# Performance work log

Hardware: AMD Instinct MI355X
Metric: run time of the kernel (lower is better)

## Reference

```python
import jax, jax.numpy as jnp
import numpy as np

B, A, E = 16384, 8, 512


def setup_inputs() -> dict:
    key = jax.random.key(0)
    ks = jax.random.split(key, 6)
    return {
        "image_features": jax.random.normal(ks[0], (B, E), dtype=jnp.float32),
        "edge_attributes": jax.random.normal(ks[1], (B, A, E), dtype=jnp.float32),
        "linear_w": jax.random.normal(ks[2], (E, 2 * E), dtype=jnp.float32) * (1.0 / np.sqrt(2 * E)),
        "linear_b": jax.random.normal(ks[3], (E,), dtype=jnp.float32) * 0.01,
        "fwd_proj": jax.random.normal(ks[4], (A, E, E), dtype=jnp.float32) * (1.0 / np.sqrt(E)),
        "bwd_proj": jax.random.normal(ks[5], (A, E, E), dtype=jnp.float32) * (1.0 / np.sqrt(E)),
        "self_weighted": jnp.ones((1, A, 1), dtype=jnp.float32),
    }


def reference(image_features, edge_attributes, linear_w, linear_b, fwd_proj, bwd_proj, self_weighted):
    # Forward attribute GNN: broadcast src over attribute axis, concat, linear(2E->E)
    src = jnp.broadcast_to(image_features[:, None, :], edge_attributes.shape)  # [B,A,E]
    x = jnp.concatenate([src, edge_attributes], axis=-1)                       # [B,A,2E]
    agg = jnp.einsum('bak,ek->bae', x, linear_w) + linear_b                    # [B,A,E]
    attr_rep = jnp.einsum('bai,aij->baj', agg, fwd_proj)                       # [B,A,E]

    # Backward attribute GNN: per-type projection, ReLU, learned weighted sum over A
    proj = jnp.einsum('bai,aij->baj', attr_rep, bwd_proj)                      # [B,A,E]
    individuals = jnp.sum(jax.nn.relu(proj) * self_weighted, axis=1)           # [B,E]
    return attr_rep, individuals
```

## Files before the change

### kernel.cpp

```cpp
#include <hip/hip_runtime.h>
#include <cstdint>
#include <cstddef>

#define NB 16384
#define NA 8
#define NE 512
#define NK 1024
#define NN 4096

typedef __bf16 bf16x8 __attribute__((ext_vector_type(8)));
typedef float  f32x4  __attribute__((ext_vector_type(4)));
typedef uint16_t u16x8 __attribute__((ext_vector_type(8)));

__device__ __forceinline__ uint16_t cvt_bf16(float f) {
    uint32_t u = __builtin_bit_cast(uint32_t, f);
    u += 0x7fffu + ((u >> 16) & 1u);
    return (uint16_t)(u >> 16);
}

__device__ __forceinline__ int swz(int row) { return (row ^ (row >> 2)) & 3; }

__device__ __forceinline__ void gl_lds16(const void* g, void* l) {
    __builtin_amdgcn_global_load_lds(
        (__attribute__((address_space(1))) void*)(void*)g,
        (__attribute__((address_space(3))) void*)l, 16, 0, 0);
}

__global__ __launch_bounds__(256) void k_tcvt(const float* __restrict__ in,
                                              uint16_t* __restrict__ out,
                                              int R, int C) {
    __shared__ float tile[32][33];
    int mat = blockIdx.z;
    int c0 = blockIdx.x * 32, r0 = blockIdx.y * 32;
    int tx = threadIdx.x & 31, ty = threadIdx.x >> 5;
    const float* src = in + (size_t)mat * R * C;
    uint16_t* dst = out + (size_t)mat * R * C;
#pragma unroll
    for (int yy = 0; yy < 4; ++yy) {
        int r = ty + yy * 8;
        tile[r][tx] = src[(size_t)(r0 + r) * C + c0 + tx];
    }
    __syncthreads();
#pragma unroll
    for (int yy = 0; yy < 4; ++yy) {
        int c = ty + yy * 8;
        dst[(size_t)(c0 + c) * R + r0 + tx] = cvt_bf16(tile[tx][c]);
    }
}

__global__ __launch_bounds__(256) void k_cvt4(const float* __restrict__ in,
                                              uint16_t* __restrict__ out, int n4) {
    int i = blockIdx.x * 256 + threadIdx.x;
    if (i >= n4) return;
    float4 v = ((const float4*)in)[i];
    ushort4 o;
    o.x = cvt_bf16(v.x); o.y = cvt_bf16(v.y); o.z = cvt_bf16(v.z); o.w = cvt_bf16(v.w);
    ((ushort4*)out)[i] = o;
}

__global__ __launch_bounds__(256) void k_bvec(const float* __restrict__ lb,
                                              const float* __restrict__ fwd,
                                              float* __restrict__ bvec) {
    int a = blockIdx.x >> 4, i0 = (blockIdx.x & 15) * 32;
    int t = threadIdx.x;
    float s0 = 0.f, s1 = 0.f;
#pragma unroll 4
    for (int i = 0; i < 32; ++i) {
        float w = lb[i0 + i];
        const float* f = fwd + ((size_t)a * NE + i0 + i) * NE;
        s0 = fmaf(w, f[t], s0);
        s1 = fmaf(w, f[t + 256], s1);
    }
    atomicAdd(&bvec[a * NE + t], s0);
    atomicAdd(&bvec[a * NE + t + 256], s1);
}

__global__ __launch_bounds__(256) void k_prep(const uint16_t* __restrict__ lwT,
                                              const uint16_t* __restrict__ fwdT,
                                              uint16_t* __restrict__ TMT) {
    __shared__ alignas(16) uint16_t lA[128 * 32];
    __shared__ alignas(16) uint16_t lB[128 * 32];
    int bz = blockIdx.x;
    int nt = bz & 31, mt = bz >> 5;
    int m0 = mt * 128, n0 = nt * 128;
    int t = threadIdx.x, lane = t & 63;
    int w = t >> 6, wm = w >> 1, wn = w & 1;
    int lr = lane & 15, lc = lane >> 4;
    int sl = swz(lr);
    f32x4 acc[4][4] = {};
    for (int k0 = 0; k0 < NE; k0 += 32) {
        __syncthreads();
#pragma unroll
        for (int p = 0; p < 2; ++p) {
            int idx = p * 256 + t;
            int row = idx >> 2, c16 = (idx & 3) ^ swz(row);
            gl_lds16(lwT + (size_t)(m0 + row) * NE + k0 + c16 * 8, lA + idx * 8);
            gl_lds16(fwdT + (size_t)(n0 + row) * NE + k0 + c16 * 8, lB + idx * 8);
        }
        __syncthreads();
        bf16x8 af[4], bfr[4];
#pragma unroll
        for (int i = 0; i < 4; ++i)
            af[i] = *(const bf16x8*)&lA[(wm * 64 + i * 16 + lr) * 32 + ((lc ^ sl) << 3)];
#pragma unroll
        for (int j = 0; j < 4; ++j)
            bfr[j] = *(const bf16x8*)&lB[(wn * 64 + j * 16 + lr) * 32 + ((lc ^ sl) << 3)];
#pragma unroll
        for (int i = 0; i < 4; ++i)
#pragma unroll
            for (int j = 0; j < 4; ++j)
                acc[i][j] = __builtin_amdgcn_mfma_f32_16x16x32_bf16(af[i], bfr[j], acc[i][j], 0, 0, 0);
    }
#pragma unroll
    for (int i = 0; i < 4; ++i) {
        int mb = m0 + wm * 64 + i * 16 + lc * 4;
#pragma unroll
        for (int j = 0; j < 4; ++j) {
            int n = n0 + wn * 64 + j * 16 + lr;
            ushort4 v;
            v.x = cvt_bf16(acc[i][j][0]);
            v.y = cvt_bf16(acc[i][j][1]);
            v.z = cvt_bf16(acc[i][j][2]);
            v.w = cvt_bf16(acc[i][j][3]);
            *(ushort4*)&TMT[(size_t)n * NK + mb] = v;
        }
    }
}

template<bool EDGEB, bool WB>
__global__ __launch_bounds__(256) void k_mm(const uint16_t* __restrict__ imgb,
                                            const float* __restrict__ edgef,
                                            const uint16_t* __restrict__ edgeb,
                                            const uint16_t* __restrict__ TMT,
                                            const float* __restrict__ bvec,
                                            float* __restrict__ attr,
                                            uint16_t* __restrict__ attrb) {
    __shared__ alignas(16) uint16_t lA[2][128 * 32];
    __shared__ alignas(16) uint16_t lB[2][128 * 32];
    int o = blockIdx.x;
    int xcd = o & 7, idx = o >> 3;
    int a = xcd, jt = idx & 3, mt = idx >> 2;
    int m0 = mt * 128, jb = jt * 128;
    int t = threadIdx.x, lane = t & 63;
    int w = t >> 6, wm = w >> 1, wn = w & 1;
    int lr = lane & 15, lc = lane >> 4;
    int sl = swz(lr);
    int srow[2], scol[2];
#pragma unroll
    for (int p = 0; p < 2; ++p) {
        int id = p * 256 + t;
        srow[p] = id >> 2;
        scol[p] = ((id & 3) ^ swz(id >> 2)) << 3;
    }
    f32x4 acc[4][4];
#pragma unroll
    for (int j = 0; j < 4; ++j) {
        float bv = bvec[a * NE + jb + wn * 64 + j * 16 + lr];
        f32x4 b4 = {bv, bv, bv, bv};
#pragma unroll
        for (int i = 0; i < 4; ++i) acc[i][j] = b4;
    }
    auto stage = [&](int buf, int s) {
        int k0 = s * 32;
        if (k0 < NE) {
#pragma unroll
            for (int p = 0; p < 2; ++p)
                gl_lds16(imgb + (size_t)(m0 + srow[p]) * NE + k0 + scol[p],
                         &lA[buf][(p * 256 + t) * 8]);
        } else if (EDGEB) {
#pragma unroll
            for (int p = 0; p < 2; ++p)
                gl_lds16(edgeb + ((size_t)(m0 + srow[p]) * NA + a) * NE + (k0 - NE) + scol[p],
                         &lA[buf][(p * 256 + t) * 8]);
        } else {
#pragma unroll
            for (int p = 0; p < 2; ++p) {
                const float* sp = edgef + ((size_t)(m0 + srow[p]) * NA + a) * NE + (k0 - NE) + scol[p];
                float4 v0 = ((const float4*)sp)[0];
                float4 v1 = ((const float4*)sp)[1];
                u16x8 ov = {cvt_bf16(v0.x), cvt_bf16(v0.y), cvt_bf16(v0.z), cvt_bf16(v0.w),
                            cvt_bf16(v1.x), cvt_bf16(v1.y), cvt_bf16(v1.z), cvt_bf16(v1.w)};
                *(u16x8*)&lA[buf][(p * 256 + t) * 8] = ov;
            }
        }
#pragma unroll
        for (int p = 0; p < 2; ++p)
            gl_lds16(TMT + (size_t)(a * NE + jb + srow[p]) * NK + k0 + scol[p],
                     &lB[buf][(p * 256 + t) * 8]);
    };
    stage(0, 0);
    __syncthreads();
    for (int s = 0; s < 32; ++s) {
        int cur = s & 1;
        if (s + 1 < 32) stage(cur ^ 1, s + 1);
        bf16x8 af[4], bfr[4];
#pragma unroll
        for (int i = 0; i < 4; ++i)
            af[i] = *(const bf16x8*)&lA[cur][(wm * 64 + i * 16 + lr) * 32 + ((lc ^ sl) << 3)];
#pragma unroll
        for (int j = 0; j < 4; ++j)
            bfr[j] = *(const bf16x8*)&lB[cur][(wn * 64 + j * 16 + lr) * 32 + ((lc ^ sl) << 3)];
#pragma unroll
        for (int i = 0; i < 4; ++i)
#pragma unroll
            for (int j = 0; j < 4; ++j)
                acc[i][j] = __builtin_amdgcn_mfma_f32_16x16x32_bf16(af[i], bfr[j], acc[i][j], 0, 0, 0);
        __syncthreads();
    }
#pragma unroll
    for (int i = 0; i < 4; ++i) {
#pragma unroll
        for (int r = 0; r < 4; ++r) {
            int bm = m0 + wm * 64 + i * 16 + lc * 4 + r;
            float* orow = attr + ((size_t)bm * NA + a) * NE + jb;
#pragma unroll
            for (int j = 0; j < 4; ++j)
                orow[wn * 64 + j * 16 + lr] = acc[i][j][r];
            if (WB) {
                uint16_t* brow = attrb + ((size_t)bm * NA + a) * NE + jb;
#pragma unroll
                for (int j = 0; j < 4; ++j)
                    brow[wn * 64 + j * 16 + lr] = cvt_bf16(acc[i][j][r]);
            }
        }
    }
}

template<bool AB>
__global__ __launch_bounds__(256) void k_ind2(const float* __restrict__ attrf,
                                              const uint16_t* __restrict__ attrb,
                                              const uint16_t* __restrict__ bwdT,
                                              const float* __restrict__ sw,
                                              float* __restrict__ ind) {
    __shared__ alignas(16) uint16_t lA[2][128 * 32];
    __shared__ alignas(16) uint16_t lB[2][128 * 32];
    int o = blockIdx.x;
    int xcd = o & 7, mt = o >> 3;
    int jt = xcd >> 1, ah = xcd & 1;
    int m0 = mt * 128, jb = jt * 128, a0 = ah * 4;
    int t = threadIdx.x, lane = t & 63;
    int w = t >> 6, wm = w >> 1, wn = w & 1;
    int lr = lane & 15, lc = lane >> 4;
    int sl = swz(lr);
    int srow[2], scol[2];
#pragma unroll
    for (int p = 0; p < 2; ++p) {
        int id = p * 256 + t;
        srow[p] = id >> 2;
        scol[p] = ((id & 3) ^ swz(id >> 2)) << 3;
    }
    f32x4 res[4][4] = {};
    f32x4 acc[4][4] = {};
    auto stage = [&](int buf, int s) {
        int a = a0 + (s >> 4), kk = (s & 15) * 32;
        if (AB) {
#pragma unroll
            for (int p = 0; p < 2; ++p)
                gl_lds16(attrb + ((size_t)(m0 + srow[p]) * NA + a) * NE + kk + scol[p],
                         &lA[buf][(p * 256 + t) * 8]);
        } else {
#pragma unroll
            for (int p = 0; p < 2; ++p) {
                const float* sp = attrf + ((size_t)(m0 + srow[p]) * NA + a) * NE + kk + scol[p];
                float4 v0 = ((const float4*)sp)[0];
                float4 v1 = ((const float4*)sp)[1];
                u16x8 ov = {cvt_bf16(v0.x), cvt_bf16(v0.y), cvt_bf16(v0.z), cvt_bf16(v0.w),
                            cvt_bf16(v1.x), cvt_bf16(v1.y), cvt_bf16(v1.z), cvt_bf16(v1.w)};
                *(u16x8*)&lA[buf][(p * 256 + t) * 8] = ov;
            }
        }
#pragma unroll
        for (int p = 0; p < 2; ++p)
            gl_lds16(bwdT + (size_t)(a * NE + jb + srow[p]) * NE + kk + scol[p],
                     &lB[buf][(p * 256 + t) * 8]);
    };
    stage(0, 0);
    __syncthreads();
    for (int s = 0; s < 64; ++s) {
        int cur = s & 1;
        if (s + 1 < 64) stage(cur ^ 1, s + 1);
        bf16x8 af[4], bfr[4];
#pragma unroll
        for (int i = 0; i < 4; ++i)
            af[i] = *(const bf16x8*)&lA[cur][(wm * 64 + i * 16 + lr) * 32 + ((lc ^ sl) << 3)];
#pragma unroll
        for (int j = 0; j < 4; ++j)
            bfr[j] = *(const bf16x8*)&lB[cur][(wn * 64 + j * 16 + lr) * 32 + ((lc ^ sl) << 3)];
#pragma unroll
        for (int i = 0; i < 4; ++i)
#pragma unroll
            for (int j = 0; j < 4; ++j)
                acc[i][j] = __builtin_amdgcn_mfma_f32_16x16x32_bf16(af[i], bfr[j], acc[i][j], 0, 0, 0);
        if ((s & 15) == 15) {
            float wa = sw[a0 + (s >> 4)];
#pragma unroll
            for (int i = 0; i < 4; ++i)
#pragma unroll
                for (int j = 0; j < 4; ++j) {
#pragma unroll
                    for (int r = 0; r < 4; ++r)
                        res[i][j][r] += wa * fmaxf(acc[i][j][r], 0.f);
                    acc[i][j] = (f32x4){0.f, 0.f, 0.f, 0.f};
                }
        }
        __syncthreads();
    }
#pragma unroll
    for (int i = 0; i < 4; ++i) {
#pragma unroll
        for (int r = 0; r < 4; ++r) {
            int bm = m0 + wm * 64 + i * 16 + lc * 4 + r;
            float* orow = ind + (size_t)bm * NE + jb;
#pragma unroll
            for (int j = 0; j < 4; ++j)
                atomicAdd(&orow[wn * 64 + j * 16 + lr], res[i][j][r]);
        }
    }
}

extern "C" void kernel_launch(void* const* d_in, const int* in_sizes, int n_in,
                              void* d_out, int out_size, void* d_ws, size_t ws_size,
                              hipStream_t stream) {
    (void)in_sizes; (void)n_in; (void)out_size;
    const float* img  = (const float*)d_in[0];
    const float* edge = (const float*)d_in[1];
    const float* lw   = (const float*)d_in[2];
    const float* lb   = (const float*)d_in[3];
    const float* fwd  = (const float*)d_in[4];
    const float* bwd  = (const float*)d_in[5];
    const float* sw   = (const float*)d_in[6];
    float* attr = (float*)d_out;
    float* ind  = attr + (size_t)NB * NA * NE;

    char* ws = (char*)d_ws;
    size_t off = 0;
    auto alloc = [&](size_t bytes) { void* p = ws + off; off += bytes; return p; };
    uint16_t* lwT  = (uint16_t*)alloc((size_t)NK * NE * 2);
    uint16_t* fwdT = (uint16_t*)alloc((size_t)NA * NE * NE * 2);
    uint16_t* bwdT = (uint16_t*)alloc((size_t)NA * NE * NE * 2);
    uint16_t* TMT  = (uint16_t*)alloc((size_t)NN * NK * 2);
    uint16_t* imgb = (uint16_t*)alloc((size_t)NB * NE * 2);
    float*    bvec = (float*)alloc((size_t)NN * 4);

    const size_t BIGB = (size_t)NB * NA * NE * 2;
    bool has_attrb = ws_size >= off + BIGB;
    uint16_t* attrb = has_attrb ? (uint16_t*)alloc(BIGB) : (uint16_t*)0;
    bool has_edgeb = ws_size >= off + BIGB;
    uint16_t* edgeb = has_edgeb ? (uint16_t*)alloc(BIGB) : (uint16_t*)0;

    hipMemsetAsync(bvec, 0, (size_t)NN * 4, stream);
    hipMemsetAsync(ind, 0, (size_t)NB * NE * 4, stream);
    k_tcvt<<<dim3(NK / 32, NE / 32, 1), 256, 0, stream>>>(lw, lwT, NE, NK);
    k_tcvt<<<dim3(NE / 32, NE / 32, NA), 256, 0, stream>>>(fwd, fwdT, NE, NE);
    k_tcvt<<<dim3(NE / 32, NE / 32, NA), 256, 0, stream>>>(bwd, bwdT, NE, NE);
    k_cvt4<<<NB * NE / 4 / 256, 256, 0, stream>>>(img, imgb, NB * NE / 4);
    if (has_edgeb)
        k_cvt4<<<NB * NA * NE / 4 / 256, 256, 0, stream>>>(edge, edgeb, NB * NA * NE / 4);
    k_bvec<<<128, 256, 0, stream>>>(lb, fwd, bvec);
    k_prep<<<(NK / 128) * (NN / 128), 256, 0, stream>>>(lwT, fwdT, TMT);

    int mm_grid = (NB / 128) * (NN / 128);
    if (has_edgeb && has_attrb)
        k_mm<true, true><<<mm_grid, 256, 0, stream>>>(imgb, edge, edgeb, TMT, bvec, attr, attrb);
    else if (has_edgeb)
        k_mm<true, false><<<mm_grid, 256, 0, stream>>>(imgb, edge, edgeb, TMT, bvec, attr, attrb);
    else if (has_attrb)
        k_mm<false, true><<<mm_grid, 256, 0, stream>>>(imgb, edge, edgeb, TMT, bvec, attr, attrb);
    else
        k_mm<false, false><<<mm_grid, 256, 0, stream>>>(imgb, edge, edgeb, TMT, bvec, attr, attrb);

    int ind_grid = (NB / 128) * (NE / 128) * 2;
    if (has_attrb)
        k_ind2<true><<<ind_grid, 256, 0, stream>>>(attr, attrb, bwdT, sw, ind);
    else
        k_ind2<false><<<ind_grid, 256, 0, stream>>>(attr, attrb, bwdT, sw, ind);
}
```

Before: 511.2 us.

## Add double-buffered async-LDS GEMM kernels with raw waitcnt/barrier pipelining

Adds new versions of the two main GEMM kernels (the fused linear+forward projection and the backward projection with ReLU and weighted sum). Both use global_load_lds double buffering, swizzled LDS addressing, and manual s_waitcnt vmcnt plus s_barrier, so the next tile's loads overlap the MFMA work on the current one. The new kernels run when the workspace holds the bf16 edge and attr copies. The intent is to hide global memory latency and cut synchronization overhead. The hand-written waitcnt counts could be wrong if the compiler schedules memory operations differently.

```diff
diff --git a/kernel.cpp b/kernel.cpp
--- a/kernel.cpp
+++ b/kernel.cpp
@@ -24,6 +24,14 @@
     __builtin_amdgcn_global_load_lds(
         (__attribute__((address_space(1))) void*)(void*)g,
         (__attribute__((address_space(3))) void*)l, 16, 0, 0);
+}
+
+__device__ __forceinline__ void waitv4() { asm volatile("s_waitcnt vmcnt(4)" ::: "memory"); }
+__device__ __forceinline__ void waitv0() { asm volatile("s_waitcnt vmcnt(0)" ::: "memory"); }
+__device__ __forceinline__ void barx()  { asm volatile("s_barrier" ::: "memory"); }
+
+__device__ __forceinline__ int cf_pos(int row, int c) {
+    return ((row >> 1) << 3) + ((((row & 1) << 2) + c) ^ ((row >> 1) & 7));
 }
 
 __global__ __launch_bounds__(256) void k_tcvt(const float* __restrict__ in,
@@ -126,6 +134,179 @@
         }
     }
 }
+
+
+__global__ __launch_bounds__(256) void k_mm2(const uint16_t* __restrict__ imgb,
+                                             const uint16_t* __restrict__ edgeb,
+                                             const uint16_t* __restrict__ TMT,
+                                             const float* __restrict__ bvec,
+                                             float* __restrict__ attr,
+                                             uint16_t* __restrict__ attrb) {
+    __shared__ alignas(16) uint16_t lA[2][128 * 32];
+    __shared__ alignas(16) uint16_t lB[2][128 * 32];
+    int o = blockIdx.x;
+    int a = o & 7, idx = o >> 3;
+    int jt = idx & 3, mt = idx >> 2;
+    int m0 = mt * 128, jb = jt * 128;
+    int t = threadIdx.x, lane = t & 63;
+    int w = t >> 6, wm = w >> 1, wn = w & 1;
+    int lr = lane & 15, lc = lane >> 4;
+    int srow[2], sc8[2];
+#pragma unroll
+    for (int p = 0; p < 2; ++p) {
+        int u = p * 256 + t;
+        int rp = u >> 3, q = (u & 7) ^ (rp & 7);
+        srow[p] = (rp << 1) | (q >> 2);
+        sc8[p] = (q & 3) << 3;
+    }
+    int aoff[4], boff[4];
+#pragma unroll
+    for (int i = 0; i < 4; ++i) {
+        aoff[i] = cf_pos(wm * 64 + i * 16 + lr, lc) * 8;
+        boff[i] = cf_pos(wn * 64 + i * 16 + lr, lc) * 8;
+    }
+    auto stage = [&](int buf, int s) {
+        int k0 = s * 32;
+#pragma unroll
+        for (int p = 0; p < 2; ++p) {
+            int u = p * 256 + t;
+            const uint16_t* asrc = (k0 < NE)
+                ? imgb + (size_t)(m0 + srow[p]) * NE + k0 + sc8[p]
+                : edgeb + ((size_t)(m0 + srow[p]) * NA + a) * NE + (k0 - NE) + sc8[p];
+            gl_lds16(asrc, &lA[buf][u * 8]);
+            gl_lds16(TMT + (size_t)(a * NE + jb + srow[p]) * NK + k0 + sc8[p],
+                     &lB[buf][u * 8]);
+        }
+    };
+    f32x4 acc[4][4] = {};
+    stage(0, 0);
+    for (int s = 0; s < 32; ++s) {
+        int cur = s & 1;
+        if (s < 31) { stage(cur ^ 1, s + 1); waitv4(); } else { waitv0(); }
+        barx();
+        bf16x8 af[4], bfr[4];
+#pragma unroll
+        for (int i = 0; i < 4; ++i) af[i] = *(const bf16x8*)&lA[cur][aoff[i]];
+#pragma unroll
+        for (int j = 0; j < 4; ++j) bfr[j] = *(const bf16x8*)&lB[cur][boff[j]];
+#pragma unroll
+        for (int i = 0; i < 4; ++i)
+#pragma unroll
+            for (int j = 0; j < 4; ++j)
+                acc[i][j] = __builtin_amdgcn_mfma_f32_16x16x32_bf16(af[i], bfr[j], acc[i][j], 0, 0, 0);
+        barx();
+    }
+#pragma unroll
+    for (int j = 0; j < 4; ++j) {
+        float bv = bvec[a * NE + jb + wn * 64 + j * 16 + lr];
+#pragma unroll
+        for (int i = 0; i < 4; ++i)
+#pragma unroll
+            for (int r = 0; r < 4; ++r)
+                acc[i][j][r] += bv;
+    }
+#pragma unroll
+    for (int i = 0; i < 4; ++i) {
+#pragma unroll
+        for (int r = 0; r < 4; ++r) {
+            int bm = m0 + wm * 64 + i * 16 + lc * 4 + r;
+            float* orow = attr + ((size_t)bm * NA + a) * NE + jb;
+            uint16_t* brow = attrb + ((size_t)bm * NA + a) * NE + jb;
+#pragma unroll
+            for (int j = 0; j < 4; ++j) {
+                orow[wn * 64 + j * 16 + lr] = acc[i][j][r];
+                brow[wn * 64 + j * 16 + lr] = cvt_bf16(acc[i][j][r]);
+            }
+        }
+    }
+}
+
+__global__ __launch_bounds__(256) void k_ind3(const uint16_t* __restrict__ attrb,
+                                              const uint16_t* __restrict__ bwdT,
+                                              const float* __restrict__ sw,
+                                              float* __restrict__ ind) {
+    __shared__ alignas(16) uint16_t lA[2][128 * 32];
+    __shared__ alignas(16) uint16_t lB[2][128 * 32];
+    int o = blockIdx.x;
+    int xcd = o & 7, mt = o >> 3;
+    int jt = xcd >> 1, ah = xcd & 1;
+    int m0 = mt * 128, jb = jt * 128, a0 = ah * 4;
+    int t = threadIdx.x, lane = t & 63;
+    int w = t >> 6, wm = w >> 1, wn = w & 1;
+    int lr = lane & 15, lc = lane >> 4;
+    int srow[2], sc8[2];
+#pragma unroll
+    for (int p = 0; p < 2; ++p) {
+        int u = p * 256 + t;
+        int rp = u >> 3, q = (u & 7) ^ (rp & 7);
+        srow[p] = (rp << 1) | (q >> 2);
+        sc8[p] = (q & 3) << 3;
+    }
+    int aoff[4], boff[4];
+#pragma unroll
+    for (int i = 0; i < 4; ++i) {
+        aoff[i] = cf_pos(wm * 64 + i * 16 + lr, lc) * 8;
+        boff[i] = cf_pos(wn * 64 + i * 16 + lr, lc) * 8;
+    }
+    float wav[4];
+#pragma unroll
+    for (int q = 0; q < 4; ++q) wav[q] = sw[a0 + q];
+    waitv0();
+    auto stage = [&](int buf, int s) {
+        int a = a0 + (s >> 4), kk = (s & 15) * 32;
+#pragma unroll
+        for (int p = 0; p < 2; ++p) {
+            int u = p * 256 + t;
+            gl_lds16(attrb + ((size_t)(m0 + srow[p]) * NA + a) * NE + kk + sc8[p],
+                     &lA[buf][u * 8]);
+            gl_lds16(bwdT + (size_t)(a * NE + jb + srow[p]) * NE + kk + sc8[p],
+                     &lB[buf][u * 8]);
+        }
+    };
+    f32x4 res[4][4] = {};
+    stage(0, 0);
+#pragma unroll
+    for (int aa = 0; aa < 4; ++aa) {
+        f32x4 acc[4][4] = {};
+        for (int ss = 0; ss < 16; ++ss) {
+            int s = aa * 16 + ss;
+            int cur = s & 1;
+            if (s < 63) { stage(cur ^ 1, s + 1); waitv4(); } else { waitv0(); }
+            barx();
+            bf16x8 af[4], bfr[4];
+#pragma unroll
+            for (int i = 0; i < 4; ++i) af[i] = *(const bf16x8*)&lA[cur][aoff[i]];
+#pragma unroll
+            for (int j = 0; j < 4; ++j) bfr[j] = *(const bf16x8*)&lB[cur][boff[j]];
+#pragma unroll
+            for (int i = 0; i < 4; ++i)
+#pragma unroll
+                for (int j = 0; j < 4; ++j)
+                    acc[i][j] = __builtin_amdgcn_mfma_f32_16x16x32_bf16(af[i], bfr[j], acc[i][j], 0, 0, 0);
+            barx();
+        }
+        float wa = wav[aa];
+#pragma unroll
+        for (int i = 0; i < 4; ++i)
+#pragma unroll
+            for (int j = 0; j < 4; ++j)
+#pragma unroll
+                for (int r = 0; r < 4; ++r)
+                    res[i][j][r] += wa * fmaxf(acc[i][j][r], 0.f);
+    }
+#pragma unroll
+    for (int i = 0; i < 4; ++i) {
+#pragma unroll
+        for (int r = 0; r < 4; ++r) {
+            int bm = m0 + wm * 64 + i * 16 + lc * 4 + r;
+            float* orow = ind + (size_t)bm * NE + jb;
+#pragma unroll
+            for (int j = 0; j < 4; ++j)
+                atomicAdd(&orow[wn * 64 + j * 16 + lr], res[i][j][r]);
+        }
+    }
+}
+
 
 template<bool EDGEB, bool WB>
 __global__ __launch_bounds__(256) void k_mm(const uint16_t* __restrict__ imgb,
@@ -360,18 +541,21 @@
     k_prep<<<(NK / 128) * (NN / 128), 256, 0, stream>>>(lwT, fwdT, TMT);
 
     int mm_grid = (NB / 128) * (NN / 128);
-    if (has_edgeb && has_attrb)
-        k_mm<true, true><<<mm_grid, 256, 0, stream>>>(imgb, edge, edgeb, TMT, bvec, attr, attrb);
-    else if (has_edgeb)
-        k_mm<true, false><<<mm_grid, 256, 0, stream>>>(imgb, edge, edgeb, TMT, bvec, attr, attrb);
-    else if (has_attrb)
-        k_mm<false, true><<<mm_grid, 256, 0, stream>>>(imgb, edge, edgeb, TMT, bvec, attr, attrb);
-    else
-        k_mm<false, false><<<mm_grid, 256, 0, stream>>>(imgb, edge, edgeb, TMT, bvec, attr, attrb);
-
     int ind_grid = (NB / 128) * (NE / 128) * 2;
-    if (has_attrb)
-        k_ind2<true><<<ind_grid, 256, 0, stream>>>(attr, attrb, bwdT, sw, ind);
-    else
-        k_ind2<false><<<ind_grid, 256, 0, stream>>>(attr, attrb, bwdT, sw, ind);
-}
+
+    if (has_edgeb && has_attrb) {
+        k_mm2<<<mm_grid, 256, 0, stream>>>(imgb, edgeb, TMT, bvec, attr, attrb);
+        k_ind3<<<ind_grid, 256, 0, stream>>>(attrb, bwdT, sw, ind);
+    } else {
+        if (has_edgeb)
+            k_mm<true, false><<<mm_grid, 256, 0, stream>>>(imgb, edge, edgeb, TMT, bvec, attr, attrb);
+        else if (has_attrb)
+            k_mm<false, true><<<mm_grid, 256, 0, stream>>>(imgb, edge, edgeb, TMT, bvec, attr, attrb);
+        else
+            k_mm<false, false><<<mm_grid, 256, 0, stream>>>(imgb, edge, edgeb, TMT, bvec, attr, attrb);
+        if (has_attrb)
+            k_ind2<true><<<ind_grid, 256, 0, stream>>>(attr, attrb, bwdT, sw, ind);
+        else
+            k_ind2<false><<<ind_grid, 256, 0, stream>>>(attr, attrb, bwdT, sw, ind);
+    }
+}
```

Result: slower. 638.7 us (+24.9%).

## Fuse edge fp32->bf16 conversion into GEMM with register prefetch and new LDS swizzle

Applied to the files above, without the earlier changes.

Drops the separate pass that converts edge_attributes to bf16 in workspace. The main GEMM now loads fp32 edge data into registers one stage ahead, converts it after the MFMAs and writes it to LDS, which removes a full read/write of the 256MB-scale edge tensor. It also switches both GEMMs to a new paired-row XOR LDS layout, moves the barrier to the top of the loop, and adds the bias after accumulation instead of before. The cost is extra VGPR pressure and VALU conversion work inside the main loop.

```diff
diff --git a/kernel.cpp b/kernel.cpp
--- a/kernel.cpp
+++ b/kernel.cpp
@@ -19,6 +19,10 @@
 }
 
 __device__ __forceinline__ int swz(int row) { return (row ^ (row >> 2)) & 3; }
+
+__device__ __forceinline__ int cf_pos(int row, int c) {
+    return ((row >> 1) << 3) + ((((row & 1) << 2) + c) ^ ((row >> 1) & 7));
+}
 
 __device__ __forceinline__ void gl_lds16(const void* g, void* l) {
     __builtin_amdgcn_global_load_lds(
@@ -127,85 +131,108 @@
     }
 }
 
-template<bool EDGEB, bool WB>
-__global__ __launch_bounds__(256) void k_mm(const uint16_t* __restrict__ imgb,
-                                            const float* __restrict__ edgef,
-                                            const uint16_t* __restrict__ edgeb,
-                                            const uint16_t* __restrict__ TMT,
-                                            const float* __restrict__ bvec,
-                                            float* __restrict__ attr,
-                                            uint16_t* __restrict__ attrb) {
+template<bool WB>
+__global__ __launch_bounds__(256) void k_mm3(const uint16_t* __restrict__ imgb,
+                                             const float* __restrict__ edge,
+                                             const uint16_t* __restrict__ TMT,
+                                             const float* __restrict__ bvec,
+                                             float* __restrict__ attr,
+                                             uint16_t* __restrict__ attrb) {
     __shared__ alignas(16) uint16_t lA[2][128 * 32];
     __shared__ alignas(16) uint16_t lB[2][128 * 32];
     int o = blockIdx.x;
-    int xcd = o & 7, idx = o >> 3;
-    int a = xcd, jt = idx & 3, mt = idx >> 2;
+    int a = o & 7, idx = o >> 3;
+    int jt = idx & 3, mt = idx >> 2;
     int m0 = mt * 128, jb = jt * 128;
     int t = threadIdx.x, lane = t & 63;
     int w = t >> 6, wm = w >> 1, wn = w & 1;
     int lr = lane & 15, lc = lane >> 4;
-    int sl = swz(lr);
-    int srow[2], scol[2];
+    int srow[2], sc8[2];
 #pragma unroll
     for (int p = 0; p < 2; ++p) {
-        int id = p * 256 + t;
-        srow[p] = id >> 2;
-        scol[p] = ((id & 3) ^ swz(id >> 2)) << 3;
-    }
-    f32x4 acc[4][4];
+        int u = p * 256 + t;
+        int rp = u >> 3, q = (u & 7) ^ (rp & 7);
+        srow[p] = (rp << 1) | (q >> 2);
+        sc8[p] = (q & 3) << 3;
+    }
+    int erow[2], ec[2], epos[2];
+#pragma unroll
+    for (int p = 0; p < 2; ++p) {
+        int u = p * 256 + t;
+        erow[p] = u >> 2; ec[p] = u & 3;
+        epos[p] = cf_pos(erow[p], ec[p]) * 8;
+    }
+    int aoff[4], boff[4];
+#pragma unroll
+    for (int i = 0; i < 4; ++i) {
+        aoff[i] = cf_pos(wm * 64 + i * 16 + lr, lc) * 8;
+        boff[i] = cf_pos(wn * 64 + i * 16 + lr, lc) * 8;
+    }
+    auto stage_img = [&](int buf, int s) {
+        int k0 = s * 32;
+#pragma unroll
+        for (int p = 0; p < 2; ++p)
+            gl_lds16(imgb + (size_t)(m0 + srow[p]) * NE + k0 + sc8[p],
+                     &lA[buf][(p * 256 + t) * 8]);
+    };
+    auto stage_tmt = [&](int buf, int s) {
+        int k0 = s * 32;
+#pragma unroll
+        for (int p = 0; p < 2; ++p)
+            gl_lds16(TMT + (size_t)(a * NE + jb + srow[p]) * NK + k0 + sc8[p],
+                     &lB[buf][(p * 256 + t) * 8]);
+    };
+    f32x4 acc[4][4] = {};
+    stage_img(0, 0);
+    stage_tmt(0, 0);
+    for (int s = 0; s < 32; ++s) {
+        int cur = s & 1, nb = cur ^ 1;
+        __syncthreads();
+        float4 er[2][2];
+        bool edgeNext = (s < 31) && (s + 1 >= 16);
+        if (s < 31) {
+            if (s + 1 < 16) {
+                stage_img(nb, s + 1);
+            } else {
+                int kk = (s + 1 - 16) * 32;
+#pragma unroll
+                for (int p = 0; p < 2; ++p) {
+                    const float* sp = edge + ((size_t)(m0 + erow[p]) * NA + a) * NE + kk + ec[p] * 8;
+                    er[p][0] = ((const float4*)sp)[0];
+                    er[p][1] = ((const float4*)sp)[1];
+                }
+            }
+            stage_tmt(nb, s + 1);
+        }
+        bf16x8 af[4], bfr[4];
+#pragma unroll
+        for (int i = 0; i < 4; ++i) af[i] = *(const bf16x8*)&lA[cur][aoff[i]];
+#pragma unroll
+        for (int j = 0; j < 4; ++j) bfr[j] = *(const bf16x8*)&lB[cur][boff[j]];
+#pragma unroll
+        for (int i = 0; i < 4; ++i)
+#pragma unroll
+            for (int j = 0; j < 4; ++j)
+                acc[i][j] = __builtin_amdgcn_mfma_f32_16x16x32_bf16(af[i], bfr[j], acc[i][j], 0, 0, 0);
+        if (edgeNext) {
+#pragma unroll
+            for (int p = 0; p < 2; ++p) {
+                u16x8 ov = {cvt_bf16(er[p][0].x), cvt_bf16(er[p][0].y),
+                            cvt_bf16(er[p][0].z), cvt_bf16(er[p][0].w),
+                            cvt_bf16(er[p][1].x), cvt_bf16(er[p][1].y),
+                            cvt_bf16(er[p][1].z), cvt_bf16(er[p][1].w)};
+                *(u16x8*)&lA[nb][epos[p]] = ov;
+            }
+        }
+    }
 #pragma unroll
     for (int j = 0; j < 4; ++j) {
         float bv = bvec[a * NE + jb + wn * 64 + j * 16 + lr];
-        f32x4 b4 = {bv, bv, bv, bv};
-#pragma unroll
-        for (int i = 0; i < 4; ++i) acc[i][j] = b4;
-    }
-    auto stage = [&](int buf, int s) {
-        int k0 = s * 32;
-        if (k0 < NE) {
-#pragma unroll
-            for (int p = 0; p < 2; ++p)
-                gl_lds16(imgb + (size_t)(m0 + srow[p]) * NE + k0 + scol[p],
-                         &lA[buf][(p * 256 + t) * 8]);
-        } else if (EDGEB) {
-#pragma unroll
-            for (int p = 0; p < 2; ++p)
-                gl_lds16(edgeb + ((size_t)(m0 + srow[p]) * NA + a) * NE + (k0 - NE) + scol[p],
-                         &lA[buf][(p * 256 + t) * 8]);
-        } else {
-#pragma unroll
-            for (int p = 0; p < 2; ++p) {
-                const float* sp = edgef + ((size_t)(m0 + srow[p]) * NA + a) * NE + (k0 - NE) + scol[p];
-                float4 v0 = ((const float4*)sp)[0];
-                float4 v1 = ((const float4*)sp)[1];
-                u16x8 ov = {cvt_bf16(v0.x), cvt_bf16(v0.y), cvt_bf16(v0.z), cvt_bf16(v0.w),
-                            cvt_bf16(v1.x), cvt_bf16(v1.y), cvt_bf16(v1.z), cvt_bf16(v1.w)};
-                *(u16x8*)&lA[buf][(p * 256 + t) * 8] = ov;
-            }
-        }
-#pragma unroll
-        for (int p = 0; p < 2; ++p)
-            gl_lds16(TMT + (size_t)(a * NE + jb + srow[p]) * NK + k0 + scol[p],
-                     &lB[buf][(p * 256 + t) * 8]);
-    };
-    stage(0, 0);
-    __syncthreads();
-    for (int s = 0; s < 32; ++s) {
-        int cur = s & 1;
-        if (s + 1 < 32) stage(cur ^ 1, s + 1);
-        bf16x8 af[4], bfr[4];
 #pragma unroll
         for (int i = 0; i < 4; ++i)
-            af[i] = *(const bf16x8*)&lA[cur][(wm * 64 + i * 16 + lr) * 32 + ((lc ^ sl) << 3)];
-#pragma unroll
-        for (int j = 0; j < 4; ++j)
-            bfr[j] = *(const bf16x8*)&lB[cur][(wn * 64 + j * 16 + lr) * 32 + ((lc ^ sl) << 3)];
-#pragma unroll
-        for (int i = 0; i < 4; ++i)
-#pragma unroll
-            for (int j = 0; j < 4; ++j)
-                acc[i][j] = __builtin_amdgcn_mfma_f32_16x16x32_bf16(af[i], bfr[j], acc[i][j], 0, 0, 0);
-        __syncthreads();
+#pragma unroll
+            for (int r = 0; r < 4; ++r)
+                acc[i][j][r] += bv;
     }
 #pragma unroll
     for (int i = 0; i < 4; ++i) {
@@ -227,7 +254,7 @@
 }
 
 template<bool AB>
-__global__ __launch_bounds__(256) void k_ind2(const float* __restrict__ attrf,
+__global__ __launch_bounds__(256) void k_ind4(const float* __restrict__ attrf,
                                               const uint16_t* __restrict__ attrb,
                                               const uint16_t* __restrict__ bwdT,
                                               const float* __restrict__ sw,
@@ -241,51 +268,62 @@
     int t = threadIdx.x, lane = t & 63;
     int w = t >> 6, wm = w >> 1, wn = w & 1;
     int lr = lane & 15, lc = lane >> 4;
-    int sl = swz(lr);
-    int srow[2], scol[2];
+    int srow[2], sc8[2];
 #pragma unroll
     for (int p = 0; p < 2; ++p) {
-        int id = p * 256 + t;
-        srow[p] = id >> 2;
-        scol[p] = ((id & 3) ^ swz(id >> 2)) << 3;
-    }
-    f32x4 res[4][4] = {};
-    f32x4 acc[4][4] = {};
+        int u = p * 256 + t;
+        int rp = u >> 3, q = (u & 7) ^ (rp & 7);
+        srow[p] = (rp << 1) | (q >> 2);
+        sc8[p] = (q & 3) << 3;
+    }
+    int erow[2], ec[2], epos[2];
+#pragma unroll
+    for (int p = 0; p < 2; ++p) {
+        int u = p * 256 + t;
+        erow[p] = u >> 2; ec[p] = u & 3;
+        epos[p] = cf_pos(erow[p], ec[p]) * 8;
+    }
+    int aoff[4], boff[4];
+#pragma unroll
+    for (int i = 0; i < 4; ++i) {
+        aoff[i] = cf_pos(wm * 64 + i * 16 + lr, lc) * 8;
+        boff[i] = cf_pos(wn * 64 + i * 16 + lr, lc) * 8;
+    }
     auto stage = [&](int buf, int s) {
-        int a = a0 + (s >> 4), kk = (s & 15) * 32;
+        int aa = a0 + (s >> 4), kk = (s & 15) * 32;
         if (AB) {
 #pragma unroll
             for (int p = 0; p < 2; ++p)
-                gl_lds16(attrb + ((size_t)(m0 + srow[p]) * NA + a) * NE + kk + scol[p],
+                gl_lds16(attrb + ((size_t)(m0 + srow[p]) * NA + aa) * NE + kk + sc8[p],
                          &lA[buf][(p * 256 + t) * 8]);
         } else {
 #pragma unroll
             for (int p = 0; p < 2; ++p) {
-                const float* sp = attrf + ((size_t)(m0 + srow[p]) * NA + a) * NE + kk + scol[p];
+                const float* sp = attrf + ((size_t)(m0 + erow[p]) * NA + aa) * NE + kk + ec[p] * 8;
                 float4 v0 = ((const float4*)sp)[0];
                 float4 v1 = ((const float4*)sp)[1];
                 u16x8 ov = {cvt_bf16(v0.x), cvt_bf16(v0.y), cvt_bf16(v0.z), cvt_bf16(v0.w),
                             cvt_bf16(v1.x), cvt_bf16(v1.y), cvt_bf16(v1.z), cvt_bf16(v1.w)};
-                *(u16x8*)&lA[buf][(p * 256 + t) * 8] = ov;
+                *(u16x8*)&lA[buf][epos[p]] = ov;
             }
         }
 #pragma unroll
         for (int p = 0; p < 2; ++p)
-            gl_lds16(bwdT + (size_t)(a * NE + jb + srow[p]) * NE + kk + scol[p],
+            gl_lds16(bwdT + (size_t)(aa * NE + jb + srow[p]) * NE + kk + sc8[p],
                      &lB[buf][(p * 256 + t) * 8]);
     };
+    f32x4 res[4][4] = {};
+    f32x4 acc[4][4] = {};
     stage(0, 0);
-    __syncthreads();
     for (int s = 0; s < 64; ++s) {
         int cur = s & 1;
-        if (s + 1 < 64) stage(cur ^ 1, s + 1);
+        __syncthreads();
+        if (s < 63) stage(cur ^ 1, s + 1);
         bf16x8 af[4], bfr[4];
 #pragma unroll
-        for (int i = 0; i < 4; ++i)
-            af[i] = *(const bf16x8*)&lA[cur][(wm * 64 + i * 16 + lr) * 32 + ((lc ^ sl) << 3)];
-#pragma unroll
-        for (int j = 0; j < 4; ++j)
-            bfr[j] = *(const bf16x8*)&lB[cur][(wn * 64 + j * 16 + lr) * 32 + ((lc ^ sl) << 3)];
+        for (int i = 0; i < 4; ++i) af[i] = *(const bf16x8*)&lA[cur][aoff[i]];
+#pragma unroll
+        for (int j = 0; j < 4; ++j) bfr[j] = *(const bf16x8*)&lB[cur][boff[j]];
 #pragma unroll
         for (int i = 0; i < 4; ++i)
 #pragma unroll
@@ -303,7 +341,6 @@
                     acc[i][j] = (f32x4){0.f, 0.f, 0.f, 0.f};
                 }
         }
-        __syncthreads();
     }
 #pragma unroll
     for (int i = 0; i < 4; ++i) {
@@ -345,8 +382,6 @@
     const size_t BIGB = (size_t)NB * NA * NE * 2;
     bool has_attrb = ws_size >= off + BIGB;
     uint16_t* attrb = has_attrb ? (uint16_t*)alloc(BIGB) : (uint16_t*)0;
-    bool has_edgeb = ws_size >= off + BIGB;
-    uint16_t* edgeb = has_edgeb ? (uint16_t*)alloc(BIGB) : (uint16_t*)0;
 
     hipMemsetAsync(bvec, 0, (size_t)NN * 4, stream);
     hipMemsetAsync(ind, 0, (size_t)NB * NE * 4, stream);
@@ -354,24 +389,17 @@
     k_tcvt<<<dim3(NE / 32, NE / 32, NA), 256, 0, stream>>>(fwd, fwdT, NE, NE);
     k_tcvt<<<dim3(NE / 32, NE / 32, NA), 256, 0, stream>>>(bwd, bwdT, NE, NE);
     k_cvt4<<<NB * NE / 4 / 256, 256, 0, stream>>>(img, imgb, NB * NE / 4);
-    if (has_edgeb)
-        k_cvt4<<<NB * NA * NE / 4 / 256, 256, 0, stream>>>(edge, edgeb, NB * NA * NE / 4);
     k_bvec<<<128, 256, 0, stream>>>(lb, fwd, bvec);
     k_prep<<<(NK / 128) * (NN / 128), 256, 0, stream>>>(lwT, fwdT, TMT);
 
     int mm_grid = (NB / 128) * (NN / 128);
-    if (has_edgeb && has_attrb)
-        k_mm<true, true><<<mm_grid, 256, 0, stream>>>(imgb, edge, edgeb, TMT, bvec, attr, attrb);
-    else if (has_edgeb)
-        k_mm<true, false><<<mm_grid, 256, 0, stream>>>(imgb, edge, edgeb, TMT, bvec, attr, attrb);
-    else if (has_attrb)
-        k_mm<false, true><<<mm_grid, 256, 0, stream>>>(imgb, edge, edgeb, TMT, bvec, attr, attrb);
-    else
-        k_mm<false, false><<<mm_grid, 256, 0, stream>>>(imgb, edge, edgeb, TMT, bvec, attr, attrb);
-
     int ind_grid = (NB / 128) * (NE / 128) * 2;
-    if (has_attrb)
-        k_ind2<true><<<ind_grid, 256, 0, stream>>>(attr, attrb, bwdT, sw, ind);
-    else
-        k_ind2<false><<<ind_grid, 256, 0, stream>>>(attr, attrb, bwdT, sw, ind);
-}
+
+    if (has_attrb) {
+        k_mm3<true><<<mm_grid, 256, 0, stream>>>(imgb, edge, TMT, bvec, attr, attrb);
+        k_ind4<true><<<ind_grid, 256, 0, stream>>>(attr, attrb, bwdT, sw, ind);
+    } else {
+        k_mm3<false><<<mm_grid, 256, 0, stream>>>(imgb, edge, TMT, bvec, attr, attrb);
+        k_ind4<false><<<ind_grid, 256, 0, stream>>>(attr, attrb, bwdT, sw, ind);
+    }
+}
```

Result: faster. 491.5 us (-3.9%).
